# Optimization experiments

Hardware: AMD Instinct MI355X
Metric: run time of the kernel (lower is better)

## Reference

```python
import jax, jax.numpy as jnp
import numpy as np

N = 50000      # total nodes
E = 500000     # edges
D = 128        # in_channels
B = 50         # graphs in batch
NPG = N // B   # nodes per graph (equal-sized graphs)
RATIO = 0.5
ALPHA = 0.6


def setup_inputs() -> dict:
    key = jax.random.key(0)
    ks = jax.random.split(key, 8)
    x = jax.random.normal(ks[0], (N, D), dtype=jnp.float32)
    edge_index = jax.random.randint(ks[1], (2, E), 0, N, dtype=jnp.int32)
    batch = jnp.repeat(jnp.arange(B, dtype=jnp.int32), NPG)  # sorted, equal blocks
    s = 1.0 / np.sqrt(D)
    # GCNConv(D,1) for structure score
    W_s = jax.random.normal(ks[2], (D, 1), dtype=jnp.float32) * s
    b_s = jnp.zeros((1,), dtype=jnp.float32)
    # Linear(D,1) for feature score
    W_f = jax.random.normal(ks[3], (1, D), dtype=jnp.float32) * s
    b_f = jnp.zeros((1,), dtype=jnp.float32)
    # GCNConv(D,D) fusion layer
    W_fu = jax.random.normal(ks[4], (D, D), dtype=jnp.float32) * s
    b_fu = jnp.zeros((D,), dtype=jnp.float32)
    return {"x": x, "edge_index": edge_index, "batch": batch,
            "W_s": W_s, "b_s": b_s, "W_f": W_f, "b_f": b_f,
            "W_fu": W_fu, "b_fu": b_fu}


def gcn_conv(x, src, dst, W, b, n):
    """PyG GCNConv: add self loops, symmetric D^-1/2 (A+I) D^-1/2 @ (xW) + b."""
    xw = x @ W                                  # [n, out]
    loop = jnp.arange(n, dtype=src.dtype)
    s = jnp.concatenate([src, loop])
    d = jnp.concatenate([dst, loop])
    deg = jax.ops.segment_sum(jnp.ones_like(s, dtype=xw.dtype), d, num_segments=n)
    dinv = jax.lax.rsqrt(jnp.maximum(deg, 1e-12))
    norm = dinv[s] * dinv[d]                    # [E+n]
    out = jax.ops.segment_sum(norm[:, None] * xw[s], d, num_segments=n)
    return out + b


def reference(x, edge_index, batch, W_s, b_s, W_f, b_f, W_fu, b_fu):
    src, dst = edge_index[0], edge_index[1]
    # fused score: alpha * structure (GCN) + (1-alpha) * feature (Linear)
    score_s = gcn_conv(x, src, dst, W_s, b_s, N)[:, 0]          # [N]
    score_f = (x @ W_f.T + b_f)[:, 0]                           # [N]
    score = jnp.tanh(ALPHA * score_s + (1.0 - ALPHA) * score_f)
    # per-graph top-k (equal-sized graphs -> dense [B, NPG] view, like the torch topk)
    k = int(np.ceil(RATIO * NPG))
    dense = score.reshape(B, NPG)
    order = jnp.argsort(-dense, axis=-1)                        # descending
    offsets = (jnp.arange(B, dtype=jnp.int32) * NPG)[:, None]
    perm = (order[:, :k].astype(jnp.int32) + offsets).reshape(-1)  # [B*k]
    # fusion conv on full graph, then gather selected nodes
    x_fused = gcn_conv(x, src, dst, W_fu, b_fu, N)              # [N, D]
    x_ae = x_fused[perm]                                        # [B*k, D]
    x_out = x_ae * score[perm][:, None]                         # multiplier == 1
    batch_out = batch[perm]
    # filter_adj: remap node ids, keep edges with both endpoints selected
    nodemap = jnp.full((N,), -1, dtype=jnp.int32).at[perm].set(
        jnp.arange(perm.shape[0], dtype=jnp.int32))
    r, c = nodemap[src], nodemap[dst]
    m = (r >= 0) & (c >= 0)
    edge_index_new = jnp.stack([r[m], c[m]], axis=0)
    return (x_out, edge_index_new, batch_out, perm, x_ae)
```

## Files before the change

### kernel.cpp

```cpp
#include <hip/hip_runtime.h>
#include <math.h>

#define N_NODES 50000
#define N_EDGES 500000
#define DIM     128
#define NGRAPH  50
#define NPGC    1000
#define KSEL    500
#define SORT_N  1024
#define NBE     489
#define NBN     49
#define GEMM_BLKS 391
#define DEG_BLKS  1954
#define DOTS_BLKS 12500
#define GATH_BLKS 6250


__global__ __launch_bounds__(256) void k1_gemm_deg(const float* __restrict__ x,
                                                   const float* __restrict__ W,
                                                   float* __restrict__ xw,
                                                   const int* __restrict__ dst,
                                                   int* __restrict__ deg) {
    __shared__ float lds[16384];
    int t = threadIdx.x;
    if (blockIdx.x >= GEMM_BLKS) {
        int e = (blockIdx.x - GEMM_BLKS) * 256 + t;
        if (e < N_EDGES) atomicAdd(&deg[dst[e]], 1);
        return;
    }
    float* Wt = lds;
    float* Xt = lds + 64 * DIM;
    int cg = t & 15;
    int ng = t >> 4;
    int node_base = blockIdx.x * 128;

    float4 acc[8][2];
    #pragma unroll
    for (int nn = 0; nn < 8; nn++) {
        acc[nn][0] = make_float4(0.f, 0.f, 0.f, 0.f);
        acc[nn][1] = make_float4(0.f, 0.f, 0.f, 0.f);
    }
    for (int half = 0; half < 2; half++) {
        const float4* Wg = (const float4*)(W + half * 64 * DIM);
        float4* Wl = (float4*)Wt;
        #pragma unroll
        for (int i = 0; i < 8; i++) {
            int f = t + i * 256;
            Wl[f] = Wg[f];
        }
        #pragma unroll
        for (int i = 0; i < 8; i++) {
            int f = t + i * 256;
            int row = f >> 4, col = f & 15;
            int node = node_base + row;
            float4 v = make_float4(0.f, 0.f, 0.f, 0.f);
            if (node < N_NODES) v = *(const float4*)&x[(size_t)node * DIM + half * 64 + col * 4];
            *(float4*)&Xt[(row << 6) + ((col ^ (row & 15)) << 2)] = v;
        }
        __syncthreads();
        #pragma unroll 2
        for (int kc = 0; kc < 16; kc++) {
            int k = kc << 2;
            float4 wa[4], wb[4];
            #pragma unroll
            for (int kk = 0; kk < 4; kk++) {
                wa[kk] = *(const float4*)&Wt[(k + kk) * DIM + (cg << 2)];
                wb[kk] = *(const float4*)&Wt[(k + kk) * DIM + (cg << 2) + 64];
            }
            int csw = (kc ^ ng) << 2;
            #pragma unroll
            for (int nn = 0; nn < 8; nn++) {
                float4 xv = *(const float4*)&Xt[((ng + (nn << 4)) << 6) + csw];
                acc[nn][0].x += xv.x * wa[0].x + xv.y * wa[1].x + xv.z * wa[2].x + xv.w * wa[3].x;
                acc[nn][0].y += xv.x * wa[0].y + xv.y * wa[1].y + xv.z * wa[2].y + xv.w * wa[3].y;
                acc[nn][0].z += xv.x * wa[0].z + xv.y * wa[1].z + xv.z * wa[2].z + xv.w * wa[3].z;
                acc[nn][0].w += xv.x * wa[0].w + xv.y * wa[1].w + xv.z * wa[2].w + xv.w * wa[3].w;
                acc[nn][1].x += xv.x * wb[0].x + xv.y * wb[1].x + xv.z * wb[2].x + xv.w * wb[3].x;
                acc[nn][1].y += xv.x * wb[0].y + xv.y * wb[1].y + xv.z * wb[2].y + xv.w * wb[3].y;
                acc[nn][1].z += xv.x * wb[0].z + xv.y * wb[1].z + xv.z * wb[2].z + xv.w * wb[3].z;
                acc[nn][1].w += xv.x * wb[0].w + xv.y * wb[1].w + xv.z * wb[2].w + xv.w * wb[3].w;
            }
        }
        __syncthreads();
    }
    #pragma unroll
    for (int nn = 0; nn < 8; nn++) {
        int node = node_base + ng + (nn << 4);
        if (node < N_NODES) {
            *(float4*)&xw[(size_t)node * DIM + (cg << 2)]      = acc[nn][0];
            *(float4*)&xw[(size_t)node * DIM + (cg << 2) + 64] = acc[nn][1];
        }
    }
}


__global__ __launch_bounds__(256) void k2_scan_dots(const int* __restrict__ deg,
                                                    int* __restrict__ rowoff,
                                                    int* __restrict__ bsumsN,
                                                    const float* __restrict__ x,
                                                    const float* __restrict__ Ws,
                                                    const float* __restrict__ Wf,
                                                    const float* __restrict__ bf,
                                                    double* __restrict__ dinv,
                                                    float* __restrict__ dinvf,
                                                    double* __restrict__ xw_s,
                                                    double* __restrict__ sf) {
    int t = threadIdx.x;
    int lane = t & 63, wid = t >> 6;
    if (blockIdx.x < NBN) {
        __shared__ int ws4[4];
        int base = blockIdx.x * 1024 + t * 4;
        int v0 = (base + 0 < N_NODES) ? deg[base + 0] : 0;
        int v1 = (base + 1 < N_NODES) ? deg[base + 1] : 0;
        int v2 = (base + 2 < N_NODES) ? deg[base + 2] : 0;
        int v3 = (base + 3 < N_NODES) ? deg[base + 3] : 0;
        int s4 = v0 + v1 + v2 + v3;
        int incl = s4;
        #pragma unroll
        for (int off = 1; off < 64; off <<= 1) {
            int u = __shfl_up(incl, off, 64);
            if (lane >= off) incl += u;
        }
        if (lane == 63) ws4[wid] = incl;
        __syncthreads();
        int woff = 0;
        #pragma unroll
        for (int w = 0; w < 4; w++) if (w < wid) woff += ws4[w];
        int excl = incl - s4 + woff;
        if (base + 0 < N_NODES) rowoff[base + 0] = excl;
        if (base + 1 < N_NODES) rowoff[base + 1] = excl + v0;
        if (base + 2 < N_NODES) rowoff[base + 2] = excl + v0 + v1;
        if (base + 3 < N_NODES) rowoff[base + 3] = excl + v0 + v1 + v2;
        if (t == 255) bsumsN[blockIdx.x] = woff + incl;
        return;
    }
    int node = (blockIdx.x - NBN) * 4 + wid;
    const float* xr = x + (size_t)node * DIM;
    double x1 = (double)xr[lane], x2 = (double)xr[lane + 64];
    double ps = x1 * (double)Ws[lane] + x2 * (double)Ws[lane + 64];
    double pf = x1 * (double)Wf[lane] + x2 * (double)Wf[lane + 64];
    for (int off = 32; off > 0; off >>= 1) {
        ps += __shfl_down(ps, off, 64);
        pf += __shfl_down(pf, off, 64);
    }
    if (lane == 0) {
        double di = 1.0 / sqrt((double)(deg[node] + 1));
        xw_s[node]  = ps;
        sf[node]    = pf + (double)bf[0];
        dinv[node]  = di;
        dinvf[node] = (float)di;
    }
}


__global__ __launch_bounds__(256) void k3_score_csr(const int* __restrict__ src,
                                                    const int* __restrict__ dst,
                                                    const double* __restrict__ dinv,
                                                    const double* __restrict__ xw_s,
                                                    double* __restrict__ score_sd,
                                                    const int* __restrict__ rowoff,
                                                    const int* __restrict__ bsumsN,
                                                    const float* __restrict__ dinvf,
                                                    int* __restrict__ cursor,
                                                    int2* __restrict__ csr) {
    __shared__ int bsN[64];
    int t = threadIdx.x;
    if (t < 64) {
        int v = (t < NBN) ? bsumsN[t] : 0;
        int incl = v;
        #pragma unroll
        for (int off = 1; off < 64; off <<= 1) {
            int u = __shfl_up(incl, off, 64);
            if (t >= off) incl += u;
        }
        bsN[t] = incl - v;
    }
    __syncthreads();
    int e = blockIdx.x * 256 + t;
    if (e >= N_EDGES) return;
    int s = src[e], d = dst[e];
    atomicAdd(&score_sd[d], dinv[s] * dinv[d] * xw_s[s]);
    int pos = rowoff[d] + bsN[d >> 10] + atomicAdd(&cursor[d], 1);
    csr[pos] = make_int2(s, __float_as_int(dinvf[s] * dinvf[d]));
}


__global__ __launch_bounds__(512) void k4_topk(const double* __restrict__ score_sd,
                                               const double* __restrict__ dinv,
                                               const double* __restrict__ xw_s,
                                               const double* __restrict__ sf,
                                               const float* __restrict__ bs,
                                               const int* __restrict__ batch,
                                               int* __restrict__ perm, int* __restrict__ nodemap,
                                               float* __restrict__ scoref_sel,
                                               float* __restrict__ out, long o2, long o3) {
    __shared__ double key[SORT_N];
    __shared__ int    idx[SORT_N];
    int g = blockIdx.x, t = threadIdx.x;
    const double A = 0.6, OMA = 1.0 - 0.6;
    double bsv = (double)bs[0];
    for (int i = t; i < SORT_N; i += 512) {
        if (i < NPGC) {
            int node = g * NPGC + i;
            double di  = dinv[node];
            double tot = score_sd[node] + di * di * xw_s[node] + bsv;
            key[i] = tanh(A * tot + OMA * sf[node]);
            idx[i] = i;
        } else { key[i] = -1e300; idx[i] = i; }
    }
    __syncthreads();
    for (int size = 2; size <= SORT_N; size <<= 1) {
        for (int stride = size >> 1; stride > 0; stride >>= 1) {
            int a = ((t & ~(stride - 1)) << 1) | (t & (stride - 1));
            int b = a | stride;
            bool descFirst = ((a & size) == 0);
            double ka = key[a], kb = key[b];
            int ia = idx[a], ib = idx[b];
            bool aAfterB = (ka < kb) || (ka == kb && ia > ib);
            if (descFirst ? aAfterB : !aAfterB) {
                key[a] = kb; key[b] = ka;
                idx[a] = ib; idx[b] = ia;
            }
            __syncthreads();
        }
    }
    for (int j = t; j < KSEL; j += 512) {
        int node = g * NPGC + idx[j];
        int pos  = g * KSEL + j;
        perm[pos]        = node;
        nodemap[node]    = pos + 1;
        scoref_sel[pos]  = (float)key[j];
        out[o2 + pos]    = (float)batch[node];
        out[o3 + pos]    = (float)node;
    }
}


__global__ __launch_bounds__(256) void k5_escan_gather(const int* __restrict__ src,
                                                       const int* __restrict__ dst,
                                                       const int* __restrict__ nodemap,
                                                       int* __restrict__ epos,
                                                       int* __restrict__ bsumsE,
                                                       const float* __restrict__ xw,
                                                       const int* __restrict__ perm,
                                                       const int* __restrict__ rowoff,
                                                       const int* __restrict__ bsumsN,
                                                       const int* __restrict__ deg,
                                                       const int2* __restrict__ csr,
                                                       const float* __restrict__ dinvf,
                                                       const float* __restrict__ scoref_sel,
                                                       const float* __restrict__ b_fu,
                                                       float* __restrict__ out, long o4) {
    int t = threadIdx.x;
    int lane = t & 63, wid = t >> 6;
    if (blockIdx.x < NBE) {
        __shared__ int ws4[4];
        int base = blockIdx.x * 1024 + t * 4;
        int v0 = 0, v1 = 0, v2 = 0, v3 = 0;
        if (base + 0 < N_EDGES) v0 = (nodemap[src[base + 0]] > 0 && nodemap[dst[base + 0]] > 0);
        if (base + 1 < N_EDGES) v1 = (nodemap[src[base + 1]] > 0 && nodemap[dst[base + 1]] > 0);
        if (base + 2 < N_EDGES) v2 = (nodemap[src[base + 2]] > 0 && nodemap[dst[base + 2]] > 0);
        if (base + 3 < N_EDGES) v3 = (nodemap[src[base + 3]] > 0 && nodemap[dst[base + 3]] > 0);
        int s4 = v0 + v1 + v2 + v3;
        int incl = s4;
        #pragma unroll
        for (int off = 1; off < 64; off <<= 1) {
            int u = __shfl_up(incl, off, 64);
            if (lane >= off) incl += u;
        }
        if (lane == 63) ws4[wid] = incl;
        __syncthreads();
        int woff = 0;
        #pragma unroll
        for (int w = 0; w < 4; w++) if (w < wid) woff += ws4[w];
        int excl = incl - s4 + woff;
        if (base + 0 < N_EDGES) epos[base + 0] = excl;
        if (base + 1 < N_EDGES) epos[base + 1] = excl + v0;
        if (base + 2 < N_EDGES) epos[base + 2] = excl + v0 + v1;
        if (base + 3 < N_EDGES) epos[base + 3] = excl + v0 + v1 + v2;
        if (t == 255) bsumsE[blockIdx.x] = woff + incl;
        return;
    }
    __shared__ int bsN[64];
    if (t < 64) {
        int v = (t < NBN) ? bsumsN[t] : 0;
        int incl = v;
        #pragma unroll
        for (int off = 1; off < 64; off <<= 1) {
            int u = __shfl_up(incl, off, 64);
            if (t >= off) incl += u;
        }
        bsN[t] = incl - v;
    }
    __syncthreads();
    int wave = (blockIdx.x - NBE) * 4 + wid;
    int p = perm[wave];
    float dpf = dinvf[p];
    int c2 = lane * 2;
    float2 v = ((const float2*)(xw + (size_t)p * DIM))[lane];
    float nself = dpf * dpf;
    float ax = nself * v.x, ay = nself * v.y;
    int beg = rowoff[p] + bsN[p >> 10], cnt = deg[p];
    int i = 0;
    for (; i + 2 <= cnt; i += 2) {
        int2 e0 = csr[beg + i];
        int2 e1 = csr[beg + i + 1];
        float2 u0 = ((const float2*)(xw + (size_t)e0.x * DIM))[lane];
        float2 u1 = ((const float2*)(xw + (size_t)e1.x * DIM))[lane];
        float n0 = __int_as_float(e0.y), n1 = __int_as_float(e1.y);
        ax += n0 * u0.x; ay += n0 * u0.y;
        ax += n1 * u1.x; ay += n1 * u1.y;
    }
    if (i < cnt) {
        int2 e0 = csr[beg + i];
        float2 u0 = ((const float2*)(xw + (size_t)e0.x * DIM))[lane];
        float n0 = __int_as_float(e0.y);
        ax += n0 * u0.x; ay += n0 * u0.y;
    }
    ax += b_fu[c2];
    ay += b_fu[c2 + 1];
    float sc = scoref_sel[wave];
    size_t ro = (size_t)wave * DIM + c2;
    out[o4 + ro]     = ax;
    out[o4 + ro + 1] = ay;
    out[ro]          = ax * sc;
    out[ro + 1]      = ay * sc;
}


__global__ __launch_bounds__(256) void k6_compact(const int* __restrict__ src,
                                                  const int* __restrict__ dst,
                                                  const int* __restrict__ nodemap,
                                                  const int* __restrict__ epos,
                                                  const int* __restrict__ bsumsE,
                                                  float* __restrict__ out_edges, long M) {
    __shared__ int bsE[512];
    int t = threadIdx.x;
    if (t < 64) {
        int carry = 0;
        #pragma unroll
        for (int c = 0; c < 8; c++) {
            int i = c * 64 + t;
            int v = (i < NBE) ? bsumsE[i] : 0;
            int incl = v;
            #pragma unroll
            for (int off = 1; off < 64; off <<= 1) {
                int u = __shfl_up(incl, off, 64);
                if (t >= off) incl += u;
            }
            if (i < 512) bsE[i] = incl - v + carry;
            carry += __shfl(incl, 63, 64);
        }
    }
    __syncthreads();
    int e = blockIdx.x * 256 + t;
    if (e >= N_EDGES) return;
    int r = nodemap[src[e]], c = nodemap[dst[e]];
    if (r > 0 && c > 0) {
        int pos = epos[e] + bsE[e >> 10];
        out_edges[pos]     = (float)(r - 1);
        out_edges[M + pos] = (float)(c - 1);
    }
}


extern "C" void kernel_launch(void* const* d_in, const int* in_sizes, int n_in,
                              void* d_out, int out_size, void* d_ws, size_t ws_size,
                              hipStream_t stream) {
    const float* x    = (const float*)d_in[0];
    const int*   ei   = (const int*)d_in[1];
    const int*   src  = ei;
    const int*   dst  = ei + N_EDGES;
    const int*   batch= (const int*)d_in[2];
    const float* W_s  = (const float*)d_in[3];
    const float* b_s  = (const float*)d_in[4];
    const float* W_f  = (const float*)d_in[5];
    const float* b_f  = (const float*)d_in[6];
    const float* W_fu = (const float*)d_in[7];
    const float* b_fu = (const float*)d_in[8];
    float* out = (float*)d_out;

    char* wsp = (char*)d_ws;
    size_t off = 0;
    auto take = [&](size_t bytes) -> char* {
        char* p = wsp + off;
        off = (off + bytes + 255) & ~(size_t)255;
        return p;
    };
    char*   zbase      = wsp;
    double* score_sd   = (double*)take((size_t)N_NODES * 8);
    int*    deg        = (int*)   take((size_t)N_NODES * 4);
    int*    cursor     = (int*)   take((size_t)N_NODES * 4);
    int*    nodemap    = (int*)   take((size_t)N_NODES * 4);
    size_t  zbytes     = off;
    double* dinv       = (double*)take((size_t)N_NODES * 8);
    double* xw_s       = (double*)take((size_t)N_NODES * 8);
    double* sf         = (double*)take((size_t)N_NODES * 8);
    float*  dinvf      = (float*) take((size_t)N_NODES * 4);
    float*  scoref_sel = (float*) take((size_t)NGRAPH * KSEL * 4);
    int*    perm       = (int*)   take((size_t)NGRAPH * KSEL * 4);
    int*    rowoff     = (int*)   take((size_t)N_NODES * 4);
    int*    epos       = (int*)   take((size_t)N_EDGES * 4);
    int*    bsumsE     = (int*)   take((size_t)1024 * 4);
    int*    bsumsN     = (int*)   take((size_t)1024 * 4);
    int2*   csr        = (int2*)  take((size_t)N_EDGES * 8);
    float*  xw         = (float*) take((size_t)N_NODES * DIM * 4);

    long M  = ((long)out_size - 6450000L) / 2;
    long o1 = 3200000L;
    long o2 = o1 + 2 * M;
    long o3 = o2 + (long)NGRAPH * KSEL;
    long o4 = o3 + (long)NGRAPH * KSEL;

    hipMemsetAsync(zbase, 0, zbytes, stream);

    k1_gemm_deg<<<GEMM_BLKS + DEG_BLKS, 256, 0, stream>>>(x, W_fu, xw, dst, deg);
    k2_scan_dots<<<NBN + DOTS_BLKS, 256, 0, stream>>>(deg, rowoff, bsumsN,
                                                      x, W_s, W_f, b_f,
                                                      dinv, dinvf, xw_s, sf);
    k3_score_csr<<<DEG_BLKS, 256, 0, stream>>>(src, dst, dinv, xw_s, score_sd,
                                               rowoff, bsumsN, dinvf, cursor, csr);
    k4_topk<<<NGRAPH, 512, 0, stream>>>(score_sd, dinv, xw_s, sf, b_s, batch,
                                        perm, nodemap, scoref_sel, out, o2, o3);
    k5_escan_gather<<<NBE + GATH_BLKS, 256, 0, stream>>>(src, dst, nodemap, epos, bsumsE,
                                                         xw, perm, rowoff, bsumsN, deg, csr,
                                                         dinvf, scoref_sel, b_fu, out, o4);
    k6_compact<<<DEG_BLKS, 256, 0, stream>>>(src, dst, nodemap, epos, bsumsE, out + o1, M);
}
```

Baseline: 245.4 us.

## Replace double atomic score scatter with CSR pull and pack dinv with xw_s

The structure-score aggregation moves from per-edge double-precision atomicAdd into a separate pull kernel that walks the CSR per destination node. CSR entries shrink from (src, norm) pairs to just src indices, and the gather recomputes the norm from dinvf. dinv and xw_s are interleaved into one double2 array so a single load serves both, and the dinv computation moves into its own blocks within k2. This removes contended FP64 atomics and halves CSR traffic, at the cost of an extra kernel launch and extra dinvf lookups in the gather.

New measurement: 228.3 us. 1.08x faster.

```diff
diff --git a/kernel.cpp b/kernel.cpp
--- a/kernel.cpp
+++ b/kernel.cpp
@@ -13,6 +13,7 @@
 #define GEMM_BLKS 391
 #define DEG_BLKS  1954
 #define DOTS_BLKS 12500
+#define NDINV     196
 #define GATH_BLKS 6250
 
 
@@ -94,22 +95,38 @@
 }
 
 
-__global__ __launch_bounds__(256) void k2_scan_dots(const int* __restrict__ deg,
-                                                    int* __restrict__ rowoff,
-                                                    int* __restrict__ bsumsN,
-                                                    const float* __restrict__ x,
-                                                    const float* __restrict__ Ws,
-                                                    const float* __restrict__ Wf,
-                                                    const float* __restrict__ bf,
-                                                    double* __restrict__ dinv,
-                                                    float* __restrict__ dinvf,
-                                                    double* __restrict__ xw_s,
-                                                    double* __restrict__ sf) {
+__global__ __launch_bounds__(256) void k2_dots_scan_dinv(const int* __restrict__ deg,
+                                                         int* __restrict__ rowoff,
+                                                         int* __restrict__ bsumsN,
+                                                         const float* __restrict__ x,
+                                                         const float* __restrict__ Ws,
+                                                         const float* __restrict__ Wf,
+                                                         const float* __restrict__ bf,
+                                                         double* __restrict__ pack,
+                                                         float* __restrict__ dinvf,
+                                                         double* __restrict__ sf) {
     int t = threadIdx.x;
     int lane = t & 63, wid = t >> 6;
-    if (blockIdx.x < NBN) {
+    int bid = blockIdx.x;
+    if (bid < DOTS_BLKS) {
+        int node = bid * 4 + wid;
+        const float* xr = x + (size_t)node * DIM;
+        double x1 = (double)xr[lane], x2 = (double)xr[lane + 64];
+        double ps = x1 * (double)Ws[lane] + x2 * (double)Ws[lane + 64];
+        double pf = x1 * (double)Wf[lane] + x2 * (double)Wf[lane + 64];
+        for (int off = 32; off > 0; off >>= 1) {
+            ps += __shfl_down(ps, off, 64);
+            pf += __shfl_down(pf, off, 64);
+        }
+        if (lane == 0) {
+            pack[2 * node + 1] = ps;
+            sf[node] = pf + (double)bf[0];
+        }
+        return;
+    }
+    if (bid < DOTS_BLKS + NBN) {
         __shared__ int ws4[4];
-        int base = blockIdx.x * 1024 + t * 4;
+        int base = (bid - DOTS_BLKS) * 1024 + t * 4;
         int v0 = (base + 0 < N_NODES) ? deg[base + 0] : 0;
         int v1 = (base + 1 < N_NODES) ? deg[base + 1] : 0;
         int v2 = (base + 2 < N_NODES) ? deg[base + 2] : 0;
@@ -131,38 +148,24 @@
         if (base + 1 < N_NODES) rowoff[base + 1] = excl + v0;
         if (base + 2 < N_NODES) rowoff[base + 2] = excl + v0 + v1;
         if (base + 3 < N_NODES) rowoff[base + 3] = excl + v0 + v1 + v2;
-        if (t == 255) bsumsN[blockIdx.x] = woff + incl;
+        if (t == 255) bsumsN[bid - DOTS_BLKS] = woff + incl;
         return;
     }
-    int node = (blockIdx.x - NBN) * 4 + wid;
-    const float* xr = x + (size_t)node * DIM;
-    double x1 = (double)xr[lane], x2 = (double)xr[lane + 64];
-    double ps = x1 * (double)Ws[lane] + x2 * (double)Ws[lane + 64];
-    double pf = x1 * (double)Wf[lane] + x2 * (double)Wf[lane + 64];
-    for (int off = 32; off > 0; off >>= 1) {
-        ps += __shfl_down(ps, off, 64);
-        pf += __shfl_down(pf, off, 64);
-    }
-    if (lane == 0) {
-        double di = 1.0 / sqrt((double)(deg[node] + 1));
-        xw_s[node]  = ps;
-        sf[node]    = pf + (double)bf[0];
-        dinv[node]  = di;
-        dinvf[node] = (float)di;
-    }
-}
-
-
-__global__ __launch_bounds__(256) void k3_score_csr(const int* __restrict__ src,
-                                                    const int* __restrict__ dst,
-                                                    const double* __restrict__ dinv,
-                                                    const double* __restrict__ xw_s,
-                                                    double* __restrict__ score_sd,
-                                                    const int* __restrict__ rowoff,
-                                                    const int* __restrict__ bsumsN,
-                                                    const float* __restrict__ dinvf,
-                                                    int* __restrict__ cursor,
-                                                    int2* __restrict__ csr) {
+    int i = (bid - DOTS_BLKS - NBN) * 256 + t;
+    if (i < N_NODES) {
+        double di = 1.0 / sqrt((double)(deg[i] + 1));
+        pack[2 * i] = di;
+        dinvf[i] = (float)di;
+    }
+}
+
+
+__global__ __launch_bounds__(256) void k3_csr(const int* __restrict__ src,
+                                              const int* __restrict__ dst,
+                                              const int* __restrict__ rowoff,
+                                              const int* __restrict__ bsumsN,
+                                              int* __restrict__ cursor,
+                                              int* __restrict__ csr) {
     __shared__ int bsN[64];
     int t = threadIdx.x;
     if (t < 64) {
@@ -178,16 +181,56 @@
     __syncthreads();
     int e = blockIdx.x * 256 + t;
     if (e >= N_EDGES) return;
-    int s = src[e], d = dst[e];
-    atomicAdd(&score_sd[d], dinv[s] * dinv[d] * xw_s[s]);
+    int d = dst[e];
     int pos = rowoff[d] + bsN[d >> 10] + atomicAdd(&cursor[d], 1);
-    csr[pos] = make_int2(s, __float_as_int(dinvf[s] * dinvf[d]));
+    csr[pos] = src[e];
+}
+
+
+__global__ __launch_bounds__(256) void k3b_score(const int* __restrict__ csr,
+                                                 const int* __restrict__ rowoff,
+                                                 const int* __restrict__ bsumsN,
+                                                 const int* __restrict__ deg,
+                                                 const double* __restrict__ pack,
+                                                 double* __restrict__ score_sd) {
+    __shared__ int bsN[64];
+    int t = threadIdx.x;
+    if (t < 64) {
+        int v = (t < NBN) ? bsumsN[t] : 0;
+        int incl = v;
+        #pragma unroll
+        for (int off = 1; off < 64; off <<= 1) {
+            int u = __shfl_up(incl, off, 64);
+            if (t >= off) incl += u;
+        }
+        bsN[t] = incl - v;
+    }
+    __syncthreads();
+    int node = blockIdx.x * 256 + t;
+    if (node >= N_NODES) return;
+    int base = rowoff[node] + bsN[node >> 10];
+    int cnt  = deg[node];
+    double acc0 = 0.0, acc1 = 0.0;
+    int i = 0;
+    for (; i + 2 <= cnt; i += 2) {
+        int s0 = csr[base + i];
+        int s1 = csr[base + i + 1];
+        double2 p0 = ((const double2*)pack)[s0];
+        double2 p1 = ((const double2*)pack)[s1];
+        acc0 += p0.x * p0.y;
+        acc1 += p1.x * p1.y;
+    }
+    if (i < cnt) {
+        int s0 = csr[base + i];
+        double2 p0 = ((const double2*)pack)[s0];
+        acc0 += p0.x * p0.y;
+    }
+    score_sd[node] = pack[2 * node] * (acc0 + acc1);
 }
 
 
 __global__ __launch_bounds__(512) void k4_topk(const double* __restrict__ score_sd,
-                                               const double* __restrict__ dinv,
-                                               const double* __restrict__ xw_s,
+                                               const double* __restrict__ pack,
                                                const double* __restrict__ sf,
                                                const float* __restrict__ bs,
                                                const int* __restrict__ batch,
@@ -202,8 +245,8 @@
     for (int i = t; i < SORT_N; i += 512) {
         if (i < NPGC) {
             int node = g * NPGC + i;
-            double di  = dinv[node];
-            double tot = score_sd[node] + di * di * xw_s[node] + bsv;
+            double2 p = ((const double2*)pack)[node];
+            double tot = score_sd[node] + p.x * p.x * p.y + bsv;
             key[i] = tanh(A * tot + OMA * sf[node]);
             idx[i] = i;
         } else { key[i] = -1e300; idx[i] = i; }
@@ -246,7 +289,7 @@
                                                        const int* __restrict__ rowoff,
                                                        const int* __restrict__ bsumsN,
                                                        const int* __restrict__ deg,
-                                                       const int2* __restrict__ csr,
+                                                       const int* __restrict__ csr,
                                                        const float* __restrict__ dinvf,
                                                        const float* __restrict__ scoref_sel,
                                                        const float* __restrict__ b_fu,
@@ -303,18 +346,18 @@
     int beg = rowoff[p] + bsN[p >> 10], cnt = deg[p];
     int i = 0;
     for (; i + 2 <= cnt; i += 2) {
-        int2 e0 = csr[beg + i];
-        int2 e1 = csr[beg + i + 1];
-        float2 u0 = ((const float2*)(xw + (size_t)e0.x * DIM))[lane];
-        float2 u1 = ((const float2*)(xw + (size_t)e1.x * DIM))[lane];
-        float n0 = __int_as_float(e0.y), n1 = __int_as_float(e1.y);
+        int s0 = csr[beg + i];
+        int s1 = csr[beg + i + 1];
+        float2 u0 = ((const float2*)(xw + (size_t)s0 * DIM))[lane];
+        float2 u1 = ((const float2*)(xw + (size_t)s1 * DIM))[lane];
+        float n0 = dinvf[s0] * dpf, n1 = dinvf[s1] * dpf;
         ax += n0 * u0.x; ay += n0 * u0.y;
         ax += n1 * u1.x; ay += n1 * u1.y;
     }
     if (i < cnt) {
-        int2 e0 = csr[beg + i];
-        float2 u0 = ((const float2*)(xw + (size_t)e0.x * DIM))[lane];
-        float n0 = __int_as_float(e0.y);
+        int s0 = csr[beg + i];
+        float2 u0 = ((const float2*)(xw + (size_t)s0 * DIM))[lane];
+        float n0 = dinvf[s0] * dpf;
         ax += n0 * u0.x; ay += n0 * u0.y;
     }
     ax += b_fu[c2];
@@ -388,13 +431,12 @@
         return p;
     };
     char*   zbase      = wsp;
-    double* score_sd   = (double*)take((size_t)N_NODES * 8);
     int*    deg        = (int*)   take((size_t)N_NODES * 4);
     int*    cursor     = (int*)   take((size_t)N_NODES * 4);
     int*    nodemap    = (int*)   take((size_t)N_NODES * 4);
     size_t  zbytes     = off;
-    double* dinv       = (double*)take((size_t)N_NODES * 8);
-    double* xw_s       = (double*)take((size_t)N_NODES * 8);
+    double* score_sd   = (double*)take((size_t)N_NODES * 8);
+    double* pack       = (double*)take((size_t)N_NODES * 16);
     double* sf         = (double*)take((size_t)N_NODES * 8);
     float*  dinvf      = (float*) take((size_t)N_NODES * 4);
     float*  scoref_sel = (float*) take((size_t)NGRAPH * KSEL * 4);
@@ -403,7 +445,7 @@
     int*    epos       = (int*)   take((size_t)N_EDGES * 4);
     int*    bsumsE     = (int*)   take((size_t)1024 * 4);
     int*    bsumsN     = (int*)   take((size_t)1024 * 4);
-    int2*   csr        = (int2*)  take((size_t)N_EDGES * 8);
+    int*    csr        = (int*)   take((size_t)N_EDGES * 4);
     float*  xw         = (float*) take((size_t)N_NODES * DIM * 4);
 
     long M  = ((long)out_size - 6450000L) / 2;
@@ -415,12 +457,12 @@
     hipMemsetAsync(zbase, 0, zbytes, stream);
 
     k1_gemm_deg<<<GEMM_BLKS + DEG_BLKS, 256, 0, stream>>>(x, W_fu, xw, dst, deg);
-    k2_scan_dots<<<NBN + DOTS_BLKS, 256, 0, stream>>>(deg, rowoff, bsumsN,
-                                                      x, W_s, W_f, b_f,
-                                                      dinv, dinvf, xw_s, sf);
-    k3_score_csr<<<DEG_BLKS, 256, 0, stream>>>(src, dst, dinv, xw_s, score_sd,
-                                               rowoff, bsumsN, dinvf, cursor, csr);
-    k4_topk<<<NGRAPH, 512, 0, stream>>>(score_sd, dinv, xw_s, sf, b_s, batch,
+    k2_dots_scan_dinv<<<DOTS_BLKS + NBN + NDINV, 256, 0, stream>>>(deg, rowoff, bsumsN,
+                                                                   x, W_s, W_f, b_f,
+                                                                   pack, dinvf, sf);
+    k3_csr<<<DEG_BLKS, 256, 0, stream>>>(src, dst, rowoff, bsumsN, cursor, csr);
+    k3b_score<<<NDINV, 256, 0, stream>>>(csr, rowoff, bsumsN, deg, pack, score_sd);
+    k4_topk<<<NGRAPH, 512, 0, stream>>>(score_sd, pack, sf, b_s, batch,
                                         perm, nodemap, scoref_sel, out, o2, o3);
     k5_escan_gather<<<NBE + GATH_BLKS, 256, 0, stream>>>(src, dst, nodemap, epos, bsumsE,
                                                          xw, perm, rowoff, bsumsN, deg, csr,
```
